# Performance work log

Hardware: AMD Instinct MI355X
Metric: run time of the kernel (lower is better)

Reference implementation:

```python
import jax, jax.numpy as jnp
import numpy as np


def _pairwise_sqdist(a, b):
    # a: [B,N,2], b: [B,M,2] -> [B,N,M] squared Euclidean distances
    a2 = jnp.sum(a * a, axis=-1)  # [B,N]
    b2 = jnp.sum(b * b, axis=-1)  # [B,M]
    ab = jnp.einsum('bnd,bmd->bnm', a, b)  # [B,N,M]
    return a2[:, :, None] + b2[:, None, :] - 2.0 * ab


def setup_inputs() -> dict:
    key = jax.random.key(0)
    k1, k2 = jax.random.split(key)
    B, N, M, D = 16, 2048, 2048, 2
    preds = jax.random.normal(k1, (B, N, D), dtype=jnp.float32)
    targs = jax.random.normal(k2, (B, M, D), dtype=jnp.float32)
    subcoef = jnp.ones((D,), dtype=jnp.float32)
    return {"preds": preds, "targs": targs, "subcoef": subcoef}


def reference(preds, targs, subcoef):
    # Bidirectional Chamfer-style NN L1 loss, faithful to NNLoss.nn_loss.
    d2 = _pairwise_sqdist(preds, targs)  # [B,N,M]

    # preds -> nearest GT (KDTree over targs queried with preds)
    nn_t = jnp.argmin(d2, axis=2)  # [B,N]
    matched_t = jnp.take_along_axis(targs, nn_t[:, :, None], axis=1)  # [B,N,2]
    move_preds_to_gt = jnp.sum(jnp.abs(preds - matched_t) * subcoef)

    # targs -> nearest pred (KDTree over preds queried with targs)
    nn_p = jnp.argmin(d2, axis=1)  # [B,M]
    matched_p = jnp.take_along_axis(preds, nn_p[:, :, None], axis=1)  # [B,M,2]
    move_gts_to_pred = jnp.sum(jnp.abs(matched_p - targs))

    return move_gts_to_pred + move_preds_to_gt
```

## Files before the change

### kernel.cpp

```cpp
#include <hip/hip_runtime.h>


constexpr int B    = 16;
constexpr int NPTS = 2048;
constexpr int BLK  = 256;
constexpr int QPT  = 4;
constexpr int QPB  = BLK * QPT;
constexpr int NGRP = 2 * B * (NPTS / QPB);
constexpr int NQ   = 2 * B * NPTS;

__global__ __launch_bounds__(BLK) void nn_partial(
    const float* __restrict__ preds, const float* __restrict__ targs,
    unsigned long long* __restrict__ ws, int S)
{
    extern __shared__ float4 sdb4[];
    const int segLen = NPTS / S;

    const int blk  = blockIdx.x;
    const int seg  = blk % S;
    const int g    = blk / S;
    const int dir  = g >> 5;
    const int b    = (g >> 1) & 15;
    const int half = g & 1;

    const float2* qb = reinterpret_cast<const float2*>(dir == 0 ? preds : targs)
                       + b * NPTS + half * QPB;
    const float2* db = reinterpret_cast<const float2*>(dir == 0 ? targs : preds)
                       + b * NPTS + seg * segLen;

    float2* sdb2 = reinterpret_cast<float2*>(sdb4);
    for (int i = threadIdx.x; i < segLen; i += BLK) sdb2[i] = db[i];
    __syncthreads();

    float m2x[QPT], m2y[QPT], best[QPT];
    int   bi[QPT];
    #pragma unroll
    for (int q = 0; q < QPT; ++q) {
        const float2 qp = qb[threadIdx.x + q * BLK];
        m2x[q] = -2.0f * qp.x;
        m2y[q] = -2.0f * qp.y;
        best[q] = 3.402823466e+38f;
        bi[q] = 0;
    }

    const int idxBase = seg * segLen;
    const int iters = segLen >> 1;
    #pragma unroll 8
    for (int i = 0; i < iters; ++i) {
        const float4 p = sdb4[i];
        const float t20 = fmaf(p.x, p.x, p.y * p.y);
        const float t21 = fmaf(p.z, p.z, p.w * p.w);
        const int i0 = idxBase + 2 * i;
        #pragma unroll
        for (int q = 0; q < QPT; ++q) {
            const float d0 = fmaf(m2x[q], p.x, fmaf(m2y[q], p.y, t20));
            if (d0 < best[q]) { best[q] = d0; bi[q] = i0; }
            const float d1 = fmaf(m2x[q], p.z, fmaf(m2y[q], p.w, t21));
            if (d1 < best[q]) { best[q] = d1; bi[q] = i0 + 1; }
        }
    }

    const int qid0 = (dir * B + b) * NPTS + half * QPB + threadIdx.x;
    unsigned long long* wseg = ws + (size_t)seg * NQ;
    #pragma unroll
    for (int q = 0; q < QPT; ++q) {
        unsigned int fb = __float_as_uint(best[q]);
        fb ^= 0x80000000u | (unsigned int)((int)fb >> 31);
        wseg[qid0 + q * BLK] =
            ((unsigned long long)fb << 32) | (unsigned int)bi[q];
    }
}

__global__ __launch_bounds__(BLK) void nn_finish(
    const float* __restrict__ preds, const float* __restrict__ targs,
    const float* __restrict__ subcoef,
    const unsigned long long* __restrict__ ws, int S,
    float* __restrict__ out)
{
    __shared__ float ssum[BLK / 64];
    const int qid = blockIdx.x * BLK + threadIdx.x;

    unsigned long long bestp = ~0ULL;
    for (int s = 0; s < S; ++s) {
        const unsigned long long v = ws[(size_t)s * NQ + qid];
        bestp = v < bestp ? v : bestp;
    }
    const int idx = (int)(unsigned int)bestp;

    const int dir = qid >> 15;
    const int rem = qid & 32767;
    const int b   = rem >> 11;
    const int n   = rem & 2047;
    const float2* qb = reinterpret_cast<const float2*>(dir == 0 ? preds : targs)
                       + b * NPTS;
    const float2* db = reinterpret_cast<const float2*>(dir == 0 ? targs : preds)
                       + b * NPTS;
    const float2 qp = qb[n];
    const float2 tp = db[idx];

    float sx = 1.0f, sy = 1.0f;
    if (dir == 0) { sx = subcoef[0]; sy = subcoef[1]; }
    float val = fabsf(qp.x - tp.x) * sx + fabsf(qp.y - tp.y) * sy;

    #pragma unroll
    for (int off = 32; off > 0; off >>= 1)
        val += __shfl_down(val, off, 64);
    if ((threadIdx.x & 63) == 0) ssum[threadIdx.x >> 6] = val;
    __syncthreads();
    if (threadIdx.x == 0) {
        float s = ssum[0];
        #pragma unroll
        for (int w = 1; w < BLK / 64; ++w) s += ssum[w];
        atomicAdd(out, s);
    }
}

extern "C" void kernel_launch(void* const* d_in, const int* in_sizes, int n_in,
                              void* d_out, int out_size, void* d_ws, size_t ws_size,
                              hipStream_t stream) {
    const float* preds   = (const float*)d_in[0];
    const float* targs   = (const float*)d_in[1];
    const float* subcoef = (const float*)d_in[2];
    float* out = (float*)d_out;
    unsigned long long* ws = (unsigned long long*)d_ws;

    const size_t per_seg = (size_t)NQ * sizeof(unsigned long long);
    int S = 1;
    if      (ws_size >= 16 * per_seg) S = 16;
    else if (ws_size >=  8 * per_seg) S = 8;
    else if (ws_size >=  4 * per_seg) S = 4;
    else if (ws_size >=  2 * per_seg) S = 2;

    hipMemsetAsync(out, 0, sizeof(float), stream);

    const int segLen = NPTS / S;
    nn_partial<<<NGRP * S, BLK, segLen * sizeof(float2), stream>>>(
        preds, targs, ws, S);
    nn_finish<<<NQ / BLK, BLK, 0, stream>>>(preds, targs, subcoef, ws, S, out);
}
```

Measured before the change: 83.48 us.

## Fuse segment argmin merge into main kernel with in-block LDS reduction

Each 1024-thread block now handles 256 queries against the full 2048-point database, with 16 wavefronts each scanning one segment and merging candidates through shared memory. This replaces the global workspace round trip of 16 partial argmin results per query and the separate finish kernel. The float atomicAdd and memset are replaced by per-block partial sums written to the workspace and a single-block deterministic reduce kernel. The grid has 256 blocks of 1024 threads, each holding about 48KB of LDS, which may limit occupancy and leave CUs idle.

```diff
diff --git a/kernel.cpp b/kernel.cpp
--- a/kernel.cpp
+++ b/kernel.cpp
@@ -1,53 +1,57 @@
 #include <hip/hip_runtime.h>
 
 
-constexpr int B    = 16;
-constexpr int NPTS = 2048;
-constexpr int BLK  = 256;
-constexpr int QPT  = 4;
-constexpr int QPB  = BLK * QPT;
-constexpr int NGRP = 2 * B * (NPTS / QPB);
-constexpr int NQ   = 2 * B * NPTS;
+constexpr int B      = 16;
+constexpr int NPTS   = 2048;
+constexpr int BLK    = 1024;
+constexpr int G      = 256;
+constexpr int S      = 16;
+constexpr int QPT    = 4;
+constexpr int SEGLEN = NPTS / S;
+constexpr int ITERS  = SEGLEN / 2;
+constexpr int NBLK   = 2 * B * (NPTS / G);
 
-__global__ __launch_bounds__(BLK) void nn_partial(
+__global__ __launch_bounds__(BLK) void nn_main(
     const float* __restrict__ preds, const float* __restrict__ targs,
-    unsigned long long* __restrict__ ws, int S)
+    const float* __restrict__ subcoef, float* __restrict__ ws_out)
 {
-    extern __shared__ float4 sdb4[];
-    const int segLen = NPTS / S;
+    __shared__ float4 sdb4[NPTS / 2];
+    __shared__ unsigned long long cand[S][G];
+    __shared__ float ssum[BLK / 64];
 
     const int blk  = blockIdx.x;
-    const int seg  = blk % S;
-    const int g    = blk / S;
-    const int dir  = g >> 5;
-    const int b    = (g >> 1) & 15;
-    const int half = g & 1;
+    const int dir  = blk >> 7;
+    const int b    = (blk >> 3) & 15;
+    const int tile = blk & 7;
 
     const float2* qb = reinterpret_cast<const float2*>(dir == 0 ? preds : targs)
-                       + b * NPTS + half * QPB;
+                       + b * NPTS + tile * G;
     const float2* db = reinterpret_cast<const float2*>(dir == 0 ? targs : preds)
-                       + b * NPTS + seg * segLen;
+                       + b * NPTS;
 
-    float2* sdb2 = reinterpret_cast<float2*>(sdb4);
-    for (int i = threadIdx.x; i < segLen; i += BLK) sdb2[i] = db[i];
-    __syncthreads();
+    const float4* db4 = reinterpret_cast<const float4*>(db);
+    for (int i = threadIdx.x; i < NPTS / 2; i += BLK) sdb4[i] = db4[i];
+
+    const int qslot = threadIdx.x & 63;
+    const int seg   = threadIdx.x >> 6;
 
     float m2x[QPT], m2y[QPT], best[QPT];
     int   bi[QPT];
     #pragma unroll
     for (int q = 0; q < QPT; ++q) {
-        const float2 qp = qb[threadIdx.x + q * BLK];
+        const float2 qp = qb[qslot + q * 64];
         m2x[q] = -2.0f * qp.x;
         m2y[q] = -2.0f * qp.y;
         best[q] = 3.402823466e+38f;
         bi[q] = 0;
     }
+    __syncthreads();
 
-    const int idxBase = seg * segLen;
-    const int iters = segLen >> 1;
+    const int pbase   = seg * ITERS;
+    const int idxBase = seg * SEGLEN;
     #pragma unroll 8
-    for (int i = 0; i < iters; ++i) {
-        const float4 p = sdb4[i];
+    for (int i = 0; i < ITERS; ++i) {
+        const float4 p = sdb4[pbase + i];
         const float t20 = fmaf(p.x, p.x, p.y * p.y);
         const float t21 = fmaf(p.z, p.z, p.w * p.w);
         const int i0 = idxBase + 2 * i;
@@ -60,47 +64,30 @@
         }
     }
 
-    const int qid0 = (dir * B + b) * NPTS + half * QPB + threadIdx.x;
-    unsigned long long* wseg = ws + (size_t)seg * NQ;
     #pragma unroll
     for (int q = 0; q < QPT; ++q) {
         unsigned int fb = __float_as_uint(best[q]);
         fb ^= 0x80000000u | (unsigned int)((int)fb >> 31);
-        wseg[qid0 + q * BLK] =
+        cand[seg][qslot + q * 64] =
             ((unsigned long long)fb << 32) | (unsigned int)bi[q];
     }
-}
+    __syncthreads();
 
-__global__ __launch_bounds__(BLK) void nn_finish(
-    const float* __restrict__ preds, const float* __restrict__ targs,
-    const float* __restrict__ subcoef,
-    const unsigned long long* __restrict__ ws, int S,
-    float* __restrict__ out)
-{
-    __shared__ float ssum[BLK / 64];
-    const int qid = blockIdx.x * BLK + threadIdx.x;
-
-    unsigned long long bestp = ~0ULL;
-    for (int s = 0; s < S; ++s) {
-        const unsigned long long v = ws[(size_t)s * NQ + qid];
-        bestp = v < bestp ? v : bestp;
+    float val = 0.0f;
+    if (threadIdx.x < G) {
+        unsigned long long bp = cand[0][threadIdx.x];
+        #pragma unroll
+        for (int s = 1; s < S; ++s) {
+            const unsigned long long v = cand[s][threadIdx.x];
+            bp = v < bp ? v : bp;
+        }
+        const int idx = (int)(unsigned int)bp;
+        const float2 qp = qb[threadIdx.x];
+        const float2 tp = db[idx];
+        float sx = 1.0f, sy = 1.0f;
+        if (dir == 0) { sx = subcoef[0]; sy = subcoef[1]; }
+        val = fabsf(qp.x - tp.x) * sx + fabsf(qp.y - tp.y) * sy;
     }
-    const int idx = (int)(unsigned int)bestp;
-
-    const int dir = qid >> 15;
-    const int rem = qid & 32767;
-    const int b   = rem >> 11;
-    const int n   = rem & 2047;
-    const float2* qb = reinterpret_cast<const float2*>(dir == 0 ? preds : targs)
-                       + b * NPTS;
-    const float2* db = reinterpret_cast<const float2*>(dir == 0 ? targs : preds)
-                       + b * NPTS;
-    const float2 qp = qb[n];
-    const float2 tp = db[idx];
-
-    float sx = 1.0f, sy = 1.0f;
-    if (dir == 0) { sx = subcoef[0]; sy = subcoef[1]; }
-    float val = fabsf(qp.x - tp.x) * sx + fabsf(qp.y - tp.y) * sy;
 
     #pragma unroll
     for (int off = 32; off > 0; off >>= 1)
@@ -111,7 +98,25 @@
         float s = ssum[0];
         #pragma unroll
         for (int w = 1; w < BLK / 64; ++w) s += ssum[w];
-        atomicAdd(out, s);
+        ws_out[blk] = s;
+    }
+}
+
+__global__ __launch_bounds__(NBLK) void nn_reduce(
+    const float* __restrict__ ws_in, float* __restrict__ out)
+{
+    __shared__ float ssum[NBLK / 64];
+    float val = ws_in[threadIdx.x];
+    #pragma unroll
+    for (int off = 32; off > 0; off >>= 1)
+        val += __shfl_down(val, off, 64);
+    if ((threadIdx.x & 63) == 0) ssum[threadIdx.x >> 6] = val;
+    __syncthreads();
+    if (threadIdx.x == 0) {
+        float s = ssum[0];
+        #pragma unroll
+        for (int w = 1; w < NBLK / 64; ++w) s += ssum[w];
+        out[0] = s;
     }
 }
 
@@ -122,19 +127,8 @@
     const float* targs   = (const float*)d_in[1];
     const float* subcoef = (const float*)d_in[2];
     float* out = (float*)d_out;
-    unsigned long long* ws = (unsigned long long*)d_ws;
+    float* ws  = (float*)d_ws;
 
-    const size_t per_seg = (size_t)NQ * sizeof(unsigned long long);
-    int S = 1;
-    if      (ws_size >= 16 * per_seg) S = 16;
-    else if (ws_size >=  8 * per_seg) S = 8;
-    else if (ws_size >=  4 * per_seg) S = 4;
-    else if (ws_size >=  2 * per_seg) S = 2;
-
-    hipMemsetAsync(out, 0, sizeof(float), stream);
-
-    const int segLen = NPTS / S;
-    nn_partial<<<NGRP * S, BLK, segLen * sizeof(float2), stream>>>(
-        preds, targs, ws, S);
-    nn_finish<<<NQ / BLK, BLK, 0, stream>>>(preds, targs, subcoef, ws, S, out);
+    nn_main<<<NBLK, BLK, 0, stream>>>(preds, targs, subcoef, ws);
+    nn_reduce<<<1, NBLK, 0, stream>>>(ws, out);
 }
```

Measured after the change: 76.06 us. -8.9%, faster.
